# Kernel optimization log

Hardware: AMD Instinct MI355X
Metric: run time of the kernel (lower is better)

## Reference

```python
import jax, jax.numpy as jnp
import numpy as np

IN_F = 5760      # padded in_features = 640 * 3 * 3 (multiple of 128)
OUT_F = 640      # padded out_features (multiple of warp_n=128)
OUT_C = 640      # original conv out_channels
RANK = 32
GROUP = 64       # 4-bit quantization group size along the K dim
KH = KW = 3
STRIDE = 1
PAD = 1


def quantize_act_w4a4(x, group=GROUP):
    """Dynamic per-token, per-group symmetric 4-bit fake-quant of activations."""
    B, L, F = x.shape
    xg = x.reshape(B, L, F // group, group)
    scale = jnp.maximum(jnp.max(jnp.abs(xg), axis=-1, keepdims=True) / 7.0, 1e-6)
    q = jnp.clip(jnp.round(xg / scale), -8.0, 7.0)
    return (q * scale).reshape(B, L, F)


def setup_inputs() -> dict:
    key = jax.random.key(0)
    k1, k2, k3, k4, k5, k6 = jax.random.split(key, 6)
    x = jax.random.normal(k1, (4, 4096, IN_F), dtype=jnp.float32)
    # 4-bit quantized weight stored as integer codes in [-8, 7] (float for GEMM)
    qweight = jax.random.randint(k2, (IN_F, OUT_F), -8, 8).astype(jnp.float32)
    # per-(group, out_channel) weight scales
    wscales = jax.random.uniform(k3, (IN_F // GROUP, OUT_F), dtype=jnp.float32) * 0.02 + 1e-3
    # SVD low-rank compensation branch (runs on unquantized activations)
    proj_down = jax.random.normal(k4, (IN_F, RANK), dtype=jnp.float32) * (1.0 / np.sqrt(IN_F))
    proj_up = jax.random.normal(k5, (RANK, OUT_F), dtype=jnp.float32) * (1.0 / np.sqrt(RANK))
    bias = jax.random.normal(k6, (OUT_F,), dtype=jnp.float32) * 0.01
    return {"x": x, "qweight": qweight, "wscales": wscales,
            "proj_down": proj_down, "proj_up": proj_up, "bias": bias,
            "N": 4, "H": 64, "W": 64}


def reference(x, qweight, wscales, proj_down, proj_up, bias, N, H, W):
    # SVDQW4A4Linear: quantized main branch + low-rank branch + bias
    x_q = quantize_act_w4a4(x)                       # [N, L, IN_F]
    w_deq = qweight * jnp.repeat(wscales, GROUP, axis=0)  # [IN_F, OUT_F]
    y = jnp.einsum('blk,kn->bln', x_q, w_deq)
    y = y + jnp.einsum('blk,kr,rn->bln', x, proj_down, proj_up)
    y = y + bias
    # slice away output-channel padding (no-op here since OUT_C == OUT_F)
    if OUT_C < y.shape[2]:
        y = y[:, :, :OUT_C]
    H_out = (H + 2 * PAD - KH) // STRIDE + 1
    W_out = (W + 2 * PAD - KW) // STRIDE + 1
    y = jnp.swapaxes(y, 1, 2).reshape(N, OUT_C, H_out, W_out)
    return y
```

## Files before the change

### kernel.cpp

```cpp
#include <hip/hip_runtime.h>

typedef unsigned short u16;
typedef unsigned int   u32;
typedef short bf16x8 __attribute__((ext_vector_type(8)));
typedef float f32x4  __attribute__((ext_vector_type(4)));

#define KT 5824
#define KI 91

__device__ __forceinline__ u16 bf16_rtne(float f) {
  u32 u = __builtin_bit_cast(u32, f);
  u += 0x7fffu + ((u >> 16) & 1u);
  return (u16)(u >> 16);
}

__device__ __forceinline__ u32 pack2(float a, float b) {
  return (u32)bf16_rtne(a) | ((u32)bf16_rtne(b) << 16);
}

__device__ __forceinline__ float fq1(float v, float inv, float s) {
  return fminf(fmaxf(rintf(v * inv), -8.f), 7.f) * s;
}

__device__ __forceinline__ void load_lds16(const void* g, void* s) {
  __builtin_amdgcn_global_load_lds((const __attribute__((address_space(1))) void*)g,
                                   (__attribute__((address_space(3))) void*)s,
                                   16, 0, 0);
}

__global__ __launch_bounds__(256) void wprep(const float* __restrict__ qw,
                                             const float* __restrict__ wsc,
                                             const float* __restrict__ pu,
                                             u16* __restrict__ Bt) {
  __shared__ u16 tile[64 * 66];
  const int tid = threadIdx.x;
  const int k0 = blockIdx.x * 64, n0 = blockIdx.y * 64;
  {
    const int n = tid & 63, kk = tid >> 6;
    const float wv = (k0 < 5760) ? wsc[(size_t)(k0 >> 6) * 640 + n0 + n] : 0.f;
    for (int p = 0; p < 16; ++p) {
      const int k = p * 4 + kk;
      const int gk = k0 + k;
      float v;
      if (gk < 5760)      v = qw[(size_t)gk * 640 + n0 + n] * wv;
      else if (gk < 5792) v = pu[(size_t)(gk - 5760) * 640 + n0 + n];
      else                v = 0.f;
      tile[k * 66 + n] = bf16_rtne(v);
    }
  }
  __syncthreads();
  {
    const int k = tid & 63, nn = tid >> 6;
    for (int p = 0; p < 16; ++p) {
      const int n2 = p * 4 + nn;
      Bt[(size_t)(n0 + n2) * KT + k0 + k] = tile[k * 66 + n2];
    }
  }
}

__global__ __launch_bounds__(256) void pdprep(const float* __restrict__ pd,
                                              u16* __restrict__ pdp) {
  const int g = blockIdx.x;
  const int f = threadIdx.x >> 6, l = threadIdx.x & 63;
  const int kc = f >> 1, nt = f & 1;
  const int k = g * 64 + kc * 32 + ((l >> 4) * 8);
  const int r = nt * 16 + (l & 15);
  u32 w[4];
  for (int jj = 0; jj < 4; ++jj)
    w[jj] = pack2(pd[(size_t)(k + 2 * jj) * 32 + r], pd[(size_t)(k + 2 * jj + 1) * 32 + r]);
  *(uint4*)(pdp + ((size_t)(g * 4 + f) * 64 + l) * 8) = make_uint4(w[0], w[1], w[2], w[3]);
}

__global__ __launch_bounds__(256) void prep(const float* __restrict__ x,
                                            const u16* __restrict__ pdp,
                                            u16* __restrict__ A) {
  __shared__ u16 xt[4][16 * 64];
  __shared__ float tl[4][512];
  const int tid = threadIdx.x;
  const int lane = tid & 63;
  const int w = tid >> 6;
  const int m0 = blockIdx.x * 16;
  const int r8 = lane >> 3, c8 = lane & 7;
  const int frow = lane & 15, fq = lane >> 4;
  const int g0   = (w == 0) ? 0 : (w == 1) ? 23 : (w == 2) ? 45 : 67;
  const int gcnt = (w == 0 || w == 3) ? 23 : 22;
  u16* xts = &xt[w][0];
  f32x4 tacc[2] = {};
  for (int gi = 0; gi < gcnt; ++gi) {
    const int g = g0 + gi;
#pragma unroll
    for (int pass = 0; pass < 2; ++pass) {
      const int row = pass * 8 + r8;
      const float* px = x + (size_t)(m0 + row) * 5760 + g * 64 + c8 * 8;
      float4 v0 = *(const float4*)px;
      float4 v1 = *(const float4*)(px + 4);
      float mx = fmaxf(fmaxf(fmaxf(fabsf(v0.x), fabsf(v0.y)), fmaxf(fabsf(v0.z), fabsf(v0.w))),
                       fmaxf(fmaxf(fabsf(v1.x), fabsf(v1.y)), fmaxf(fabsf(v1.z), fabsf(v1.w))));
      mx = fmaxf(mx, __shfl_xor(mx, 1, 64));
      mx = fmaxf(mx, __shfl_xor(mx, 2, 64));
      mx = fmaxf(mx, __shfl_xor(mx, 4, 64));
      const float s = fmaxf(mx / 7.0f, 1e-6f);
      const float inv = 1.0f / s;
      uint4 qv = make_uint4(pack2(fq1(v0.x, inv, s), fq1(v0.y, inv, s)),
                            pack2(fq1(v0.z, inv, s), fq1(v0.w, inv, s)),
                            pack2(fq1(v1.x, inv, s), fq1(v1.y, inv, s)),
                            pack2(fq1(v1.z, inv, s), fq1(v1.w, inv, s)));
      *(uint4*)(A + (size_t)(m0 + row) * KT + g * 64 + c8 * 8) = qv;
      uint4 rv = make_uint4(pack2(v0.x, v0.y), pack2(v0.z, v0.w),
                            pack2(v1.x, v1.y), pack2(v1.z, v1.w));
      *(uint4*)(&xts[row * 64 + ((c8 ^ r8) * 8)]) = rv;
    }
#pragma unroll
    for (int kc = 0; kc < 2; ++kc) {
      bf16x8 xf = *(const bf16x8*)&xts[frow * 64 + (((kc * 4 + fq) ^ (frow & 7)) * 8)];
#pragma unroll
      for (int nt = 0; nt < 2; ++nt) {
        bf16x8 pf = *(const bf16x8*)(pdp + ((size_t)(g * 4 + kc * 2 + nt) * 64 + lane) * 8);
        tacc[nt] = __builtin_amdgcn_mfma_f32_16x16x32_bf16(xf, pf, tacc[nt], 0, 0, 0);
      }
    }
  }
#pragma unroll
  for (int nt = 0; nt < 2; ++nt)
#pragma unroll
    for (int r0 = 0; r0 < 4; ++r0)
      tl[w][(fq * 4 + r0) * 32 + nt * 16 + frow] = tacc[nt][r0];
  __syncthreads();
  if (w == 0) {
    const int m = lane >> 2, rb = (lane & 3) * 8;
    u32 pk[4];
    for (int jj = 0; jj < 4; ++jj) {
      const int i0 = m * 32 + rb + 2 * jj;
      float sa = tl[0][i0] + tl[1][i0] + tl[2][i0] + tl[3][i0];
      float sb = tl[0][i0 + 1] + tl[1][i0 + 1] + tl[2][i0 + 1] + tl[3][i0 + 1];
      pk[jj] = (u32)bf16_rtne(sa) | ((u32)bf16_rtne(sb) << 16);
    }
    *(uint4*)(A + (size_t)(m0 + m) * KT + 5760 + rb) = make_uint4(pk[0], pk[1], pk[2], pk[3]);
  } else if (w == 1) {
    const int m = lane >> 2, rb = (lane & 3) * 8;
    *(uint4*)(A + (size_t)(m0 + m) * KT + 5792 + rb) = make_uint4(0, 0, 0, 0);
  }
}

__global__ __launch_bounds__(256, 2) void gemm_kernel(const u16* __restrict__ A,
                                                      const u16* __restrict__ Bt,
                                                      const float* __restrict__ bias,
                                                      float* __restrict__ out) {
  __shared__ u16 As[128 * 64];
  __shared__ u16 Bs[160 * 64];
  const int tid = threadIdx.x;
  const int lane = tid & 63;
  const int w = tid >> 6;
  const int wm = w & 1, wn = w >> 1;
  const int lin = blockIdx.x;
  const int g = (lin & 7) * 64 + (lin >> 3);
  const int n0 = (g >> 7) * 160;
  const int m0 = (g & 127) * 128;

  const int srow = lane >> 3;
  const int sch = (lane & 7) ^ srow;
  const u16* ga = A  + (size_t)(m0 + w * 32 + srow) * KT + sch * 8;
  const u16* gb = Bt + (size_t)(n0 + w * 40 + srow) * KT + sch * 8;

  const int frow = lane & 15, fq = lane >> 4;
  f32x4 acc[4][5] = {};

  for (int kt = 0; kt < KI; ++kt) {
    const u16* gak = ga + kt * 64;
    const u16* gbk = gb + kt * 64;
#pragma unroll
    for (int i = 0; i < 4; ++i)
      load_lds16(gak + (size_t)(i * 8) * KT, &As[(w * 32 + i * 8) * 64]);
#pragma unroll
    for (int i = 0; i < 5; ++i)
      load_lds16(gbk + (size_t)(i * 8) * KT, &Bs[(w * 40 + i * 8) * 64]);
    __syncthreads();
#pragma unroll
    for (int kc = 0; kc < 2; ++kc) {
      const int ch = kc * 4 + fq;
      const int sw = (ch ^ (frow & 7)) * 8;
      bf16x8 af[4], bfr[5];
#pragma unroll
      for (int mt = 0; mt < 4; ++mt)
        af[mt] = *(const bf16x8*)&As[(wm * 64 + mt * 16 + frow) * 64 + sw];
#pragma unroll
      for (int nt = 0; nt < 5; ++nt)
        bfr[nt] = *(const bf16x8*)&Bs[(wn * 80 + nt * 16 + frow) * 64 + sw];
#pragma unroll
      for (int mt = 0; mt < 4; ++mt)
#pragma unroll
        for (int nt = 0; nt < 5; ++nt)
          acc[mt][nt] = __builtin_amdgcn_mfma_f32_16x16x32_bf16(bfr[nt], af[mt], acc[mt][nt], 0, 0, 0);
    }
    __syncthreads();
  }

  const int batch = m0 >> 12;
  float* outb = out + (size_t)batch * (640 * 4096) + (m0 & 4095) + wm * 64 + frow;
  const int cb = n0 + wn * 80 + fq * 4;
#pragma unroll
  for (int nt = 0; nt < 5; ++nt) {
#pragma unroll
    for (int r = 0; r < 4; ++r) {
      const int c = cb + nt * 16 + r;
      const float bv = bias[c];
      float* op = outb + (size_t)c * 4096;
#pragma unroll
      for (int mt = 0; mt < 4; ++mt)
        op[mt * 16] = acc[mt][nt][r] + bv;
    }
  }
}

extern "C" void kernel_launch(void* const* d_in, const int* in_sizes, int n_in,
                              void* d_out, int out_size, void* d_ws, size_t ws_size,
                              hipStream_t stream) {
  const float* x    = (const float*)d_in[0];
  const float* qw   = (const float*)d_in[1];
  const float* wsc  = (const float*)d_in[2];
  const float* pd   = (const float*)d_in[3];
  const float* pu   = (const float*)d_in[4];
  const float* bias = (const float*)d_in[5];
  float* out = (float*)d_out;
  char* wsb = (char*)d_ws;
  u16* A   = (u16*)wsb;
  u16* Bt  = (u16*)(wsb + 190840832);
  u16* pdp = (u16*)(wsb + 198295552);

  wprep<<<dim3(91, 10), dim3(256), 0, stream>>>(qw, wsc, pu, Bt);
  pdprep<<<dim3(90), dim3(256), 0, stream>>>(pd, pdp);
  prep<<<dim3(1024), dim3(256), 0, stream>>>(x, pdp, A);
  gemm_kernel<<<dim3(512), dim3(256), 0, stream>>>(A, Bt, bias, out);
}
```

Measured before the change: 723.6 us.

## Triple-buffer GEMM LDS tiles with prefetch and a larger 256x160 block tile

Rewrites the GEMM main loop to use three LDS buffers, so global-to-LDS loads run two K-steps ahead. Those loads are interleaved between the MFMA phases, using raw s_barrier, explicit vmcnt waits and s_setprio around the MFMA clusters. The block grows to 512 threads covering a 256x160 output tile, which halves the grid and improves B-tile reuse. The intent is to hide global memory latency behind matrix math and cut per-tile synchronization stalls. The cost is roughly 159KB of LDS per block, which limits residency to one block per CU, and barrier and waitcnt handling that is harder to get right.

Result: slower. 858.0 us (+18.6%).

```diff
diff --git a/kernel.cpp b/kernel.cpp
--- a/kernel.cpp
+++ b/kernel.cpp
@@ -142,57 +142,101 @@
   }
 }
 
-__global__ __launch_bounds__(256, 2) void gemm_kernel(const u16* __restrict__ A,
+__global__ __launch_bounds__(512, 2) void gemm_kernel(const u16* __restrict__ A,
                                                       const u16* __restrict__ Bt,
                                                       const float* __restrict__ bias,
                                                       float* __restrict__ out) {
-  __shared__ u16 As[128 * 64];
-  __shared__ u16 Bs[160 * 64];
+  __shared__ u16 As[3][256 * 64];
+  __shared__ u16 Bs[3][160 * 64];
   const int tid = threadIdx.x;
   const int lane = tid & 63;
   const int w = tid >> 6;
-  const int wm = w & 1, wn = w >> 1;
+  const int wm = w & 3, wn = w >> 2;
   const int lin = blockIdx.x;
-  const int g = (lin & 7) * 64 + (lin >> 3);
-  const int n0 = (g >> 7) * 160;
-  const int m0 = (g & 127) * 128;
+  const int g = (lin & 7) * 32 + (lin >> 3);
+  const int n0 = (g >> 6) * 160;
+  const int m0 = (g & 63) * 256;
 
   const int srow = lane >> 3;
   const int sch = (lane & 7) ^ srow;
   const u16* ga = A  + (size_t)(m0 + w * 32 + srow) * KT + sch * 8;
-  const u16* gb = Bt + (size_t)(n0 + w * 40 + srow) * KT + sch * 8;
+  const u16* gb = Bt + (size_t)(n0 + srow) * KT + sch * 8;
 
   const int frow = lane & 15, fq = lane >> 4;
   f32x4 acc[4][5] = {};
 
+#pragma unroll
+  for (int t = 0; t < 2; ++t) {
+    const u16* gak = ga + t * 64;
+    const u16* gbk = gb + t * 64;
+#pragma unroll
+    for (int i = 0; i < 4; ++i)
+      load_lds16(gak + (size_t)(i * 8) * KT, &As[t][(w * 32 + i * 8) * 64]);
+    load_lds16(gbk + (size_t)(w * 8) * KT, &Bs[t][(w * 8) * 64]);
+    load_lds16(gbk + (size_t)((w + 8) * 8) * KT, &Bs[t][((w + 8) * 8) * 64]);
+    if (w < 4)
+      load_lds16(gbk + (size_t)((w + 16) * 8) * KT, &Bs[t][((w + 16) * 8) * 64]);
+  }
+
+  int c = 0;
   for (int kt = 0; kt < KI; ++kt) {
-    const u16* gak = ga + kt * 64;
-    const u16* gbk = gb + kt * 64;
-#pragma unroll
-    for (int i = 0; i < 4; ++i)
-      load_lds16(gak + (size_t)(i * 8) * KT, &As[(w * 32 + i * 8) * 64]);
-#pragma unroll
-    for (int i = 0; i < 5; ++i)
-      load_lds16(gbk + (size_t)(i * 8) * KT, &Bs[(w * 40 + i * 8) * 64]);
-    __syncthreads();
+    const int nxt = (c >= 1) ? c - 1 : c + 2;
+    const bool pf = (kt + 2 < KI);
+    const u16* gan = ga + (size_t)(kt + 2) * 64;
+    const u16* gbn = gb + (size_t)(kt + 2) * 64;
+    if (kt == KI - 1) asm volatile("s_waitcnt vmcnt(0)" ::: "memory");
+    else              asm volatile("s_waitcnt vmcnt(6)" ::: "memory");
+    __builtin_amdgcn_s_barrier();
+    const u16* as = &As[c][0];
+    const u16* bs = &Bs[c][0];
 #pragma unroll
     for (int kc = 0; kc < 2; ++kc) {
-      const int ch = kc * 4 + fq;
-      const int sw = (ch ^ (frow & 7)) * 8;
-      bf16x8 af[4], bfr[5];
-#pragma unroll
-      for (int mt = 0; mt < 4; ++mt)
-        af[mt] = *(const bf16x8*)&As[(wm * 64 + mt * 16 + frow) * 64 + sw];
+      const int sw = ((kc * 4 + fq) ^ (frow & 7)) * 8;
+      if (pf) {
+        if (kc == 0) {
+          load_lds16(gan, &As[nxt][(w * 32) * 64]);
+          load_lds16(gan + (size_t)(8) * KT, &As[nxt][(w * 32 + 8) * 64]);
+        } else {
+          load_lds16(gbn + (size_t)(w * 8) * KT, &Bs[nxt][(w * 8) * 64]);
+          load_lds16(gbn + (size_t)((w + 8) * 8) * KT, &Bs[nxt][((w + 8) * 8) * 64]);
+        }
+      }
+      bf16x8 bfr[5];
 #pragma unroll
       for (int nt = 0; nt < 5; ++nt)
-        bfr[nt] = *(const bf16x8*)&Bs[(wn * 80 + nt * 16 + frow) * 64 + sw];
-#pragma unroll
-      for (int mt = 0; mt < 4; ++mt)
-#pragma unroll
-        for (int nt = 0; nt < 5; ++nt)
-          acc[mt][nt] = __builtin_amdgcn_mfma_f32_16x16x32_bf16(bfr[nt], af[mt], acc[mt][nt], 0, 0, 0);
-    }
-    __syncthreads();
+        bfr[nt] = *(const bf16x8*)&bs[(wn * 80 + nt * 16 + frow) * 64 + sw];
+      bf16x8 af0 = *(const bf16x8*)&as[(wm * 64 + frow) * 64 + sw];
+      bf16x8 af1 = *(const bf16x8*)&as[(wm * 64 + 16 + frow) * 64 + sw];
+      __builtin_amdgcn_s_barrier();
+      __builtin_amdgcn_s_setprio(1);
+#pragma unroll
+      for (int nt = 0; nt < 5; ++nt) {
+        acc[0][nt] = __builtin_amdgcn_mfma_f32_16x16x32_bf16(bfr[nt], af0, acc[0][nt], 0, 0, 0);
+        acc[1][nt] = __builtin_amdgcn_mfma_f32_16x16x32_bf16(bfr[nt], af1, acc[1][nt], 0, 0, 0);
+      }
+      __builtin_amdgcn_s_setprio(0);
+      __builtin_amdgcn_s_barrier();
+      if (pf) {
+        if (kc == 0) {
+          load_lds16(gan + (size_t)(16) * KT, &As[nxt][(w * 32 + 16) * 64]);
+          load_lds16(gan + (size_t)(24) * KT, &As[nxt][(w * 32 + 24) * 64]);
+        } else if (w < 4) {
+          load_lds16(gbn + (size_t)((w + 16) * 8) * KT, &Bs[nxt][((w + 16) * 8) * 64]);
+        }
+      }
+      bf16x8 af2 = *(const bf16x8*)&as[(wm * 64 + 32 + frow) * 64 + sw];
+      bf16x8 af3 = *(const bf16x8*)&as[(wm * 64 + 48 + frow) * 64 + sw];
+      __builtin_amdgcn_s_barrier();
+      __builtin_amdgcn_s_setprio(1);
+#pragma unroll
+      for (int nt = 0; nt < 5; ++nt) {
+        acc[2][nt] = __builtin_amdgcn_mfma_f32_16x16x32_bf16(bfr[nt], af2, acc[2][nt], 0, 0, 0);
+        acc[3][nt] = __builtin_amdgcn_mfma_f32_16x16x32_bf16(bfr[nt], af3, acc[3][nt], 0, 0, 0);
+      }
+      __builtin_amdgcn_s_setprio(0);
+      if (kc == 0) __builtin_amdgcn_s_barrier();
+    }
+    c = (c + 1 == 3) ? 0 : c + 1;
   }
 
   const int batch = m0 >> 12;
@@ -202,9 +246,9 @@
   for (int nt = 0; nt < 5; ++nt) {
 #pragma unroll
     for (int r = 0; r < 4; ++r) {
-      const int c = cb + nt * 16 + r;
-      const float bv = bias[c];
-      float* op = outb + (size_t)c * 4096;
+      const int cc = cb + nt * 16 + r;
+      const float bv = bias[cc];
+      float* op = outb + (size_t)cc * 4096;
 #pragma unroll
       for (int mt = 0; mt < 4; ++mt)
         op[mt * 16] = acc[mt][nt][r] + bv;
@@ -230,5 +274,5 @@
   wprep<<<dim3(91, 10), dim3(256), 0, stream>>>(qw, wsc, pu, Bt);
   pdprep<<<dim3(90), dim3(256), 0, stream>>>(pd, pdp);
   prep<<<dim3(1024), dim3(256), 0, stream>>>(x, pdp, A);
-  gemm_kernel<<<dim3(512), dim3(256), 0, stream>>>(A, Bt, bias, out);
-}
+  gemm_kernel<<<dim3(256), dim3(512), 0, stream>>>(A, Bt, bias, out);
+}
```

## Fuse activation quantization and low-rank down-projection into the main GEMM

Applied to the files above, without the earlier changes.

Removes the separate prep kernel and the large bf16 A workspace. The activation tile is now quantized on the fly inside the GEMM, and the x·proj_down product is accumulated alongside it, then written into the extra K columns of the LDS tile in the last iteration. The block tile changes to 64 rows by all 640 columns, and B fragments are read straight from global memory instead of being staged in LDS. This saves the round trip through the A buffer, but each block now rereads all of B from global/L2 with no LDS reuse, and only 256 blocks run.

After: 1.010 ms. 39.6% more time.

```diff
diff --git a/kernel.cpp b/kernel.cpp
--- a/kernel.cpp
+++ b/kernel.cpp
@@ -6,7 +6,6 @@
 typedef float f32x4  __attribute__((ext_vector_type(4)));
 
 #define KT 5824
-#define KI 91
 
 __device__ __forceinline__ u16 bf16_rtne(float f) {
   u32 u = __builtin_bit_cast(u32, f);
@@ -20,12 +19,6 @@
 
 __device__ __forceinline__ float fq1(float v, float inv, float s) {
   return fminf(fmaxf(rintf(v * inv), -8.f), 7.f) * s;
-}
-
-__device__ __forceinline__ void load_lds16(const void* g, void* s) {
-  __builtin_amdgcn_global_load_lds((const __attribute__((address_space(1))) void*)g,
-                                   (__attribute__((address_space(3))) void*)s,
-                                   16, 0, 0);
 }
 
 __global__ __launch_bounds__(256) void wprep(const float* __restrict__ qw,
@@ -71,143 +64,106 @@
   *(uint4*)(pdp + ((size_t)(g * 4 + f) * 64 + l) * 8) = make_uint4(w[0], w[1], w[2], w[3]);
 }
 
-__global__ __launch_bounds__(256) void prep(const float* __restrict__ x,
-                                            const u16* __restrict__ pdp,
-                                            u16* __restrict__ A) {
-  __shared__ u16 xt[4][16 * 64];
-  __shared__ float tl[4][512];
+__global__ __launch_bounds__(512, 2) void fgemm(const float* __restrict__ x,
+                                                const u16* __restrict__ Bt,
+                                                const u16* __restrict__ pdp,
+                                                const float* __restrict__ bias,
+                                                float* __restrict__ out) {
+  __shared__ u16 Aq[64 * 64];
+  __shared__ u16 xr[64 * 64];
   const int tid = threadIdx.x;
   const int lane = tid & 63;
   const int w = tid >> 6;
-  const int m0 = blockIdx.x * 16;
+  const int wm = w & 1, wn = w >> 1;
+  const int m0 = blockIdx.x * 64;
   const int r8 = lane >> 3, c8 = lane & 7;
+  const int srow = w * 8 + r8;
   const int frow = lane & 15, fq = lane >> 4;
-  const int g0   = (w == 0) ? 0 : (w == 1) ? 23 : (w == 2) ? 45 : 67;
-  const int gcnt = (w == 0 || w == 3) ? 23 : 22;
-  u16* xts = &xt[w][0];
-  f32x4 tacc[2] = {};
-  for (int gi = 0; gi < gcnt; ++gi) {
-    const int g = g0 + gi;
-#pragma unroll
-    for (int pass = 0; pass < 2; ++pass) {
-      const int row = pass * 8 + r8;
-      const float* px = x + (size_t)(m0 + row) * 5760 + g * 64 + c8 * 8;
-      float4 v0 = *(const float4*)px;
-      float4 v1 = *(const float4*)(px + 4);
-      float mx = fmaxf(fmaxf(fmaxf(fabsf(v0.x), fabsf(v0.y)), fmaxf(fabsf(v0.z), fabsf(v0.w))),
-                       fmaxf(fmaxf(fabsf(v1.x), fabsf(v1.y)), fmaxf(fabsf(v1.z), fabsf(v1.w))));
+  const int mtt = w & 3, rt = w >> 2;
+
+  f32x4 acc[2][10] = {};
+  f32x4 tacc = {};
+
+  const float* px = x + (size_t)(m0 + srow) * 5760 + c8 * 8;
+  float4 v0 = *(const float4*)px;
+  float4 v1 = *(const float4*)(px + 4);
+
+#pragma unroll 1
+  for (int kt = 0; kt < 91; ++kt) {
+    if (kt < 90) {
+      float4 c0 = v0, c1 = v1;
+      if (kt < 89) {
+        const float* pn = px + (size_t)(kt + 1) * 64;
+        v0 = *(const float4*)pn;
+        v1 = *(const float4*)(pn + 4);
+      }
+      float mx = fmaxf(fmaxf(fmaxf(fabsf(c0.x), fabsf(c0.y)), fmaxf(fabsf(c0.z), fabsf(c0.w))),
+                       fmaxf(fmaxf(fabsf(c1.x), fabsf(c1.y)), fmaxf(fabsf(c1.z), fabsf(c1.w))));
       mx = fmaxf(mx, __shfl_xor(mx, 1, 64));
       mx = fmaxf(mx, __shfl_xor(mx, 2, 64));
       mx = fmaxf(mx, __shfl_xor(mx, 4, 64));
       const float s = fmaxf(mx / 7.0f, 1e-6f);
       const float inv = 1.0f / s;
-      uint4 qv = make_uint4(pack2(fq1(v0.x, inv, s), fq1(v0.y, inv, s)),
-                            pack2(fq1(v0.z, inv, s), fq1(v0.w, inv, s)),
-                            pack2(fq1(v1.x, inv, s), fq1(v1.y, inv, s)),
-                            pack2(fq1(v1.z, inv, s), fq1(v1.w, inv, s)));
-      *(uint4*)(A + (size_t)(m0 + row) * KT + g * 64 + c8 * 8) = qv;
-      uint4 rv = make_uint4(pack2(v0.x, v0.y), pack2(v0.z, v0.w),
-                            pack2(v1.x, v1.y), pack2(v1.z, v1.w));
-      *(uint4*)(&xts[row * 64 + ((c8 ^ r8) * 8)]) = rv;
-    }
+      uint4 qv = make_uint4(pack2(fq1(c0.x, inv, s), fq1(c0.y, inv, s)),
+                            pack2(fq1(c0.z, inv, s), fq1(c0.w, inv, s)),
+                            pack2(fq1(c1.x, inv, s), fq1(c1.y, inv, s)),
+                            pack2(fq1(c1.z, inv, s), fq1(c1.w, inv, s)));
+      *(uint4*)&Aq[srow * 64 + ((c8 ^ r8) * 8)] = qv;
+      uint4 rv = make_uint4(pack2(c0.x, c0.y), pack2(c0.z, c0.w),
+                            pack2(c1.x, c1.y), pack2(c1.z, c1.w));
+      *(uint4*)&xr[srow * 64 + ((c8 ^ r8) * 8)] = rv;
+    } else {
+      const int col = rt * 16 + frow;
+      const int ch = col >> 3, co = col & 7;
+      const int zc = 4 + (frow & 3);
 #pragma unroll
-    for (int kc = 0; kc < 2; ++kc) {
-      bf16x8 xf = *(const bf16x8*)&xts[frow * 64 + (((kc * 4 + fq) ^ (frow & 7)) * 8)];
-#pragma unroll
-      for (int nt = 0; nt < 2; ++nt) {
-        bf16x8 pf = *(const bf16x8*)(pdp + ((size_t)(g * 4 + kc * 2 + nt) * 64 + lane) * 8);
-        tacc[nt] = __builtin_amdgcn_mfma_f32_16x16x32_bf16(xf, pf, tacc[nt], 0, 0, 0);
+      for (int r0 = 0; r0 < 4; ++r0) {
+        const int rr = mtt * 16 + fq * 4 + r0;
+        Aq[rr * 64 + ((ch ^ (rr & 7)) * 8) + co] = bf16_rtne(tacc[r0]);
+        *(uint4*)&Aq[rr * 64 + ((zc ^ (rr & 7)) * 8)] = make_uint4(0, 0, 0, 0);
       }
     }
-  }
-#pragma unroll
-  for (int nt = 0; nt < 2; ++nt)
-#pragma unroll
-    for (int r0 = 0; r0 < 4; ++r0)
-      tl[w][(fq * 4 + r0) * 32 + nt * 16 + frow] = tacc[nt][r0];
-  __syncthreads();
-  if (w == 0) {
-    const int m = lane >> 2, rb = (lane & 3) * 8;
-    u32 pk[4];
-    for (int jj = 0; jj < 4; ++jj) {
-      const int i0 = m * 32 + rb + 2 * jj;
-      float sa = tl[0][i0] + tl[1][i0] + tl[2][i0] + tl[3][i0];
-      float sb = tl[0][i0 + 1] + tl[1][i0 + 1] + tl[2][i0 + 1] + tl[3][i0 + 1];
-      pk[jj] = (u32)bf16_rtne(sa) | ((u32)bf16_rtne(sb) << 16);
-    }
-    *(uint4*)(A + (size_t)(m0 + m) * KT + 5760 + rb) = make_uint4(pk[0], pk[1], pk[2], pk[3]);
-  } else if (w == 1) {
-    const int m = lane >> 2, rb = (lane & 3) * 8;
-    *(uint4*)(A + (size_t)(m0 + m) * KT + 5792 + rb) = make_uint4(0, 0, 0, 0);
-  }
-}
+    asm volatile("s_waitcnt lgkmcnt(0)" ::: "memory");
+    __builtin_amdgcn_s_barrier();
 
-__global__ __launch_bounds__(256, 2) void gemm_kernel(const u16* __restrict__ A,
-                                                      const u16* __restrict__ Bt,
-                                                      const float* __restrict__ bias,
-                                                      float* __restrict__ out) {
-  __shared__ u16 As[128 * 64];
-  __shared__ u16 Bs[160 * 64];
-  const int tid = threadIdx.x;
-  const int lane = tid & 63;
-  const int w = tid >> 6;
-  const int wm = w & 1, wn = w >> 1;
-  const int lin = blockIdx.x;
-  const int g = (lin & 7) * 64 + (lin >> 3);
-  const int n0 = (g >> 7) * 160;
-  const int m0 = (g & 127) * 128;
-
-  const int srow = lane >> 3;
-  const int sch = (lane & 7) ^ srow;
-  const u16* ga = A  + (size_t)(m0 + w * 32 + srow) * KT + sch * 8;
-  const u16* gb = Bt + (size_t)(n0 + w * 40 + srow) * KT + sch * 8;
-
-  const int frow = lane & 15, fq = lane >> 4;
-  f32x4 acc[4][5] = {};
-
-  for (int kt = 0; kt < KI; ++kt) {
-    const u16* gak = ga + kt * 64;
-    const u16* gbk = gb + kt * 64;
-#pragma unroll
-    for (int i = 0; i < 4; ++i)
-      load_lds16(gak + (size_t)(i * 8) * KT, &As[(w * 32 + i * 8) * 64]);
-#pragma unroll
-    for (int i = 0; i < 5; ++i)
-      load_lds16(gbk + (size_t)(i * 8) * KT, &Bs[(w * 40 + i * 8) * 64]);
-    __syncthreads();
+    const size_t kOff = (size_t)kt * 64;
 #pragma unroll
     for (int kc = 0; kc < 2; ++kc) {
       const int ch = kc * 4 + fq;
       const int sw = (ch ^ (frow & 7)) * 8;
-      bf16x8 af[4], bfr[5];
+      bf16x8 bfr[10];
 #pragma unroll
-      for (int mt = 0; mt < 4; ++mt)
-        af[mt] = *(const bf16x8*)&As[(wm * 64 + mt * 16 + frow) * 64 + sw];
+      for (int nt = 0; nt < 10; ++nt)
+        bfr[nt] = *(const bf16x8*)(Bt + (size_t)(wn * 160 + nt * 16 + frow) * KT + kOff + ch * 8);
+      bf16x8 af0 = *(const bf16x8*)&Aq[(wm * 32 + frow) * 64 + sw];
+      bf16x8 af1 = *(const bf16x8*)&Aq[(wm * 32 + 16 + frow) * 64 + sw];
 #pragma unroll
-      for (int nt = 0; nt < 5; ++nt)
-        bfr[nt] = *(const bf16x8*)&Bs[(wn * 80 + nt * 16 + frow) * 64 + sw];
-#pragma unroll
-      for (int mt = 0; mt < 4; ++mt)
-#pragma unroll
-        for (int nt = 0; nt < 5; ++nt)
-          acc[mt][nt] = __builtin_amdgcn_mfma_f32_16x16x32_bf16(bfr[nt], af[mt], acc[mt][nt], 0, 0, 0);
+      for (int nt = 0; nt < 10; ++nt) {
+        acc[0][nt] = __builtin_amdgcn_mfma_f32_16x16x32_bf16(bfr[nt], af0, acc[0][nt], 0, 0, 0);
+        acc[1][nt] = __builtin_amdgcn_mfma_f32_16x16x32_bf16(bfr[nt], af1, acc[1][nt], 0, 0, 0);
+      }
+      if (kt < 90) {
+        bf16x8 xf = *(const bf16x8*)&xr[(mtt * 16 + frow) * 64 + sw];
+        bf16x8 pf = *(const bf16x8*)(pdp + ((size_t)(kt * 4 + kc * 2 + rt) * 64 + lane) * 8);
+        tacc = __builtin_amdgcn_mfma_f32_16x16x32_bf16(xf, pf, tacc, 0, 0, 0);
+      }
     }
-    __syncthreads();
+    asm volatile("s_waitcnt lgkmcnt(0)" ::: "memory");
+    __builtin_amdgcn_s_barrier();
   }
 
   const int batch = m0 >> 12;
-  float* outb = out + (size_t)batch * (640 * 4096) + (m0 & 4095) + wm * 64 + frow;
-  const int cb = n0 + wn * 80 + fq * 4;
+  float* outb = out + (size_t)batch * (640 * 4096) + (m0 & 4095) + wm * 32 + frow;
+  const int cb = wn * 160 + fq * 4;
 #pragma unroll
-  for (int nt = 0; nt < 5; ++nt) {
+  for (int nt = 0; nt < 10; ++nt) {
 #pragma unroll
     for (int r = 0; r < 4; ++r) {
       const int c = cb + nt * 16 + r;
       const float bv = bias[c];
       float* op = outb + (size_t)c * 4096;
-#pragma unroll
-      for (int mt = 0; mt < 4; ++mt)
-        op[mt * 16] = acc[mt][nt][r] + bv;
+      op[0]  = acc[0][nt][r] + bv;
+      op[16] = acc[1][nt][r] + bv;
     }
   }
 }
@@ -223,12 +179,10 @@
   const float* bias = (const float*)d_in[5];
   float* out = (float*)d_out;
   char* wsb = (char*)d_ws;
-  u16* A   = (u16*)wsb;
-  u16* Bt  = (u16*)(wsb + 190840832);
-  u16* pdp = (u16*)(wsb + 198295552);
+  u16* Bt  = (u16*)wsb;
+  u16* pdp = (u16*)(wsb + 7454720);
 
   wprep<<<dim3(91, 10), dim3(256), 0, stream>>>(qw, wsc, pu, Bt);
   pdprep<<<dim3(90), dim3(256), 0, stream>>>(pd, pdp);
-  prep<<<dim3(1024), dim3(256), 0, stream>>>(x, pdp, A);
-  gemm_kernel<<<dim3(512), dim3(256), 0, stream>>>(A, Bt, bias, out);
+  fgemm<<<dim3(256), dim3(512), 0, stream>>>(x, Bt, pdp, bias, out);
 }
```
